# Performance work log

Measured on AMD Instinct MI355X. Metric: run time of the kernel, lower is better.

## Reference

```python
import jax, jax.numpy as jnp
import numpy as np

WINDOW_SIZE = 16


def _gru_seq(x, Wih, Whh, bih, bhh):
    # x: (T, in); Wih: (in, 3H); Whh: (H, 3H); torch gate order r,z,n
    H = Whh.shape[0]
    pre = x @ Wih + bih  # (T, 3H)
    def step(h, pi):
        ph = h @ Whh + bhh
        ri, zi, ni = jnp.split(pi, 3)
        rh, zh, nh = jnp.split(ph, 3)
        r = jax.nn.sigmoid(ri + rh)
        z = jax.nn.sigmoid(zi + zh)
        n = jnp.tanh(ni + r * nh)
        hn = (1.0 - z) * n + z * h
        return hn, hn
    _, ys = jax.lax.scan(step, jnp.zeros((H,), x.dtype), pre)
    return ys


def _bigru(x, Wih, Whh, bih, bhh):
    f = _gru_seq(x, Wih[0], Whh[0], bih[0], bhh[0])
    b = _gru_seq(x[::-1], Wih[1], Whh[1], bih[1], bhh[1])[::-1]
    return jnp.concatenate([f, b], axis=-1)


def setup_inputs() -> dict:
    key = jax.random.key(0)
    ks = iter(jax.random.split(key, 64))
    T, S = 512, 32
    VFD, HID, WED, VOCAB = 1024, 512, 300, 10000
    HH = HID // 2
    def p(*shape):
        return jax.random.normal(next(ks), shape, jnp.float32) * 0.05
    return dict(
        video=jax.random.normal(next(ks), (T, VFD), jnp.float32),
        text=jax.random.randint(next(ks), (S,), 0, VOCAB),
        vp_W=p(VFD, HID), vp_b=p(HID),
        vgru_Wih=p(2, HID, 3 * HH), vgru_Whh=p(2, HH, 3 * HH),
        vgru_bih=p(2, 3 * HH), vgru_bhh=p(2, 3 * HH),
        emb=p(VOCAB, WED),
        tp_W=p(WED, HID), tp_b=p(HID),
        tgru_Wih=p(2, HID, 3 * HH), tgru_Whh=p(2, HH, 3 * HH),
        tgru_bih=p(2, 3 * HH), tgru_bhh=p(2, 3 * HH),
        cma_Wq=p(HID, HID), cma_bq=p(HID), cma_Wk=p(HID, HID), cma_bk=p(HID), cma_v=p(HID),
        cm_gru_Wih=p(2 * HID, 3 * HID), cm_gru_Whh=p(HID, 3 * HID),
        cm_gru_bih=p(3 * HID), cm_gru_bhh=p(3 * HID),
        si_Wq=p(HID, HID), si_bq=p(HID), si_Wk=p(HID, HID), si_bk=p(HID), si_v=p(HID),
        si_gru_Wih=p(2 * HID, 3 * HID), si_gru_Whh=p(HID, 3 * HID),
        si_gru_bih=p(3 * HID), si_gru_bhh=p(3 * HID),
        wp_W1=p(HID, HID), wp_b1=p(HID), wp_v=p(HID),
        cp_W1=p(2 * HID, HID), cp_b1=p(HID), cp_v=p(HID),
    )


def reference(video, text, vp_W, vp_b, vgru_Wih, vgru_Whh, vgru_bih, vgru_bhh,
              emb, tp_W, tp_b, tgru_Wih, tgru_Whh, tgru_bih, tgru_bhh,
              cma_Wq, cma_bq, cma_Wk, cma_bk, cma_v,
              cm_gru_Wih, cm_gru_Whh, cm_gru_bih, cm_gru_bhh,
              si_Wq, si_bq, si_Wk, si_bk, si_v,
              si_gru_Wih, si_gru_Whh, si_gru_bih, si_gru_bhh,
              wp_W1, wp_b1, wp_v, cp_W1, cp_b1, cp_v):
    T = video.shape[0]
    # encoders (dropout is identity in eval)
    H_v = _bigru(video @ vp_W + vp_b, vgru_Wih, vgru_Whh, vgru_bih, vgru_bhh)  # (T, HID)
    H_s = _bigru(emb[text] @ tp_W + tp_b, tgru_Wih, tgru_Whh, tgru_bih, tgru_bhh)  # (S, HID)
    # cross-modal additive attention: score = v . tanh(Wq q + Wk k)
    e = jnp.tanh((H_v @ cma_Wq + cma_bq)[:, None, :] + (H_s @ cma_Wk + cma_bk)[None, :, :])  # (T,S,HID)
    w = jax.nn.softmax(e @ cma_v, axis=1)  # (T,S)
    h_s_bar = w @ H_s  # (T, HID)
    # cross gating (linear layers defined but unused in original forward)
    h_v_t = jax.nn.relu(H_v) * h_s_bar
    h_s_t = jax.nn.relu(h_s_bar) * h_v_t
    h_r = _gru_seq(jnp.concatenate([h_v_t, h_s_t], axis=1),
                   cm_gru_Wih, cm_gru_Whh, cm_gru_bih, cm_gru_bhh)  # (T, HID)
    # self interactor: row i attends over X[i:] -> mask j >= i
    e2 = jnp.tanh((h_r @ si_Wq + si_bq)[:, None, :] + (h_r @ si_Wk + si_bk)[None, :, :])  # (T,T,HID)
    s2 = e2 @ si_v  # (T,T)
    mask = jnp.arange(T)[None, :] >= jnp.arange(T)[:, None]
    s2 = jnp.where(mask, s2, jnp.asarray(-1e30, s2.dtype))
    att = jax.nn.softmax(s2, axis=1) @ h_r  # (T, HID)
    h_d = _gru_seq(jnp.concatenate([h_r, att], axis=1),
                   si_gru_Wih, si_gru_Whh, si_gru_bih, si_gru_bhh)  # (T, HID)
    # segment localizer; torch nn.Softmax() on (S,1) acts on axis=1 (size 1) -> all ones (faithful)
    wlogits = jnp.tanh(H_s @ wp_W1 + wp_b1) @ wp_v  # (S,)
    wts = jax.nn.softmax(wlogits[:, None], axis=1)  # (S,1) == ones
    h_o = jnp.sum(H_s * wts, axis=0)  # (HID,)
    cat = jnp.concatenate([h_d, jnp.broadcast_to(h_o, h_d.shape)], axis=1)  # (T, 2*HID)
    frame_scores = jnp.tanh(cat @ cp_W1 + cp_b1) @ cp_v  # (T,)
    n_win = T - WINDOW_SIZE + 1
    window_starts = jnp.arange(n_win)
    window_scores = frame_scores[:n_win]
    return (window_scores, window_starts)
```

## Files before the change

### kernel.cpp

```cpp
#include <hip/hip_runtime.h>
#include <hip/hip_bf16.h>
#include <cstdint>

#define DEV __device__ __forceinline__

typedef unsigned short ushort;
typedef __attribute__((ext_vector_type(8))) short bf16x8;
typedef __attribute__((ext_vector_type(4))) float f32x4;

DEV float fsig(float x) { return 1.f / (1.f + __expf(-x)); }
DEV float ftanh(float x) { return 1.f - 2.f / (1.f + __expf(2.f * x)); }
DEV ushort f2bu(float f) {
  __hip_bfloat16 h = __float2bfloat16(f);
  return *(ushort*)&h;
}
DEV float b2f(ushort u) { return __uint_as_float((uint32_t)u << 16); }

template <int CTRL>
DEV float dpp_add(float v) {
  int x = __builtin_amdgcn_update_dpp(0, __float_as_int(v), CTRL, 0xF, 0xF, true);
  return v + __int_as_float(x);
}
template <int TPU>
DEV float dpp_reduce(float v) {
  v = dpp_add<0xB1>(v);
  v = dpp_add<0x4E>(v);
  if (TPU >= 8) v = dpp_add<0x141>(v);
  if (TPU >= 16) v = dpp_add<0x140>(v);
  return v;
}

__global__ __launch_bounds__(256)
void mfma_gemm(const ushort* __restrict__ A, const ushort* __restrict__ BT,
               const float* __restrict__ bias, void* __restrict__ Cout,
               int M, int N, int K, int ldc, int flags) {
  const int wave = threadIdx.x >> 6, lane = threadIdx.x & 63;
  const int m0 = blockIdx.y * 64 + wave * 16;
  const int n0 = blockIdx.x * 64;
  const int r = lane & 15, quad = lane >> 4;
  f32x4 acc[4] = {};
  const int arow = (m0 + r < M) ? (m0 + r) : 0;
  const ushort* ap = A + (size_t)arow * K + quad * 8;
  const ushort* bp = BT + (size_t)(n0 + r) * K + quad * 8;
#pragma unroll 2
  for (int k0 = 0; k0 < K; k0 += 32) {
    bf16x8 a = *(const bf16x8*)(ap + k0);
#pragma unroll
    for (int t = 0; t < 4; ++t) {
      bf16x8 b = *(const bf16x8*)(bp + (size_t)t * 16 * K + k0);
      acc[t] = __builtin_amdgcn_mfma_f32_16x16x32_bf16(a, b, acc[t], 0, 0, 0);
    }
  }
#pragma unroll
  for (int t = 0; t < 4; ++t) {
    const int col = n0 + t * 16 + r;
    const float bs = bias ? bias[col] : 0.f;
#pragma unroll
    for (int e = 0; e < 4; ++e) {
      const int row = m0 + quad * 4 + e;
      if (row < M) {
        float v = acc[t][e] + bs;
        if (flags & 1) v = ftanh(v);
        if (flags & 2)
          ((ushort*)Cout)[(size_t)row * ldc + col] = f2bu(v);
        else
          ((float*)Cout)[(size_t)row * ldc + col] = v;
      }
    }
  }
}

struct TDesc {
  const float* src;
  ushort* db;
  float* df;
  int K, N, Kp;
};
struct PrepArgs {
  TDesc d[19];
  int n;
};

__global__ __launch_bounds__(256)
void prep_kernel(PrepArgs pa) {
  int rem = blockIdx.x;
  int di = 0;
  TDesc d{};
  for (; di < pa.n; ++di) {
    d = pa.d[di];
    int t = ((d.N + 31) >> 5) * ((d.Kp + 31) >> 5);
    if (rem < t) break;
    rem -= t;
  }
  if (di == pa.n) return;
  const int ntx = (d.Kp + 31) >> 5;
  const int ty = rem / ntx, tx = rem % ntx;
  __shared__ float t32[32][33];
  const int lx = threadIdx.x & 31, ly = threadIdx.x >> 5;
#pragma unroll
  for (int p = 0; p < 4; ++p) {
    int k = tx * 32 + ly + 8 * p;
    int n = ty * 32 + lx;
    t32[ly + 8 * p][lx] = (k < d.K && n < d.N) ? d.src[(size_t)k * d.N + n] : 0.f;
  }
  __syncthreads();
#pragma unroll
  for (int p = 0; p < 4; ++p) {
    int n = ty * 32 + ly + 8 * p;
    int k = tx * 32 + lx;
    if (n < d.N && k < d.Kp) {
      float v = t32[lx][ly + 8 * p];
      if (d.df)
        d.df[(size_t)n * d.Kp + k] = v;
      else
        d.db[(size_t)n * d.Kp + k] = f2bu(v);
    }
  }
}

__global__ void cast_kernel(const float* __restrict__ in,
                            ushort* __restrict__ out, int n) {
  int i = (blockIdx.x * 256 + threadIdx.x) * 4;
  if (i + 3 < n) {
    float4 v = *(const float4*)(in + i);
    out[i] = f2bu(v.x);
    out[i + 1] = f2bu(v.y);
    out[i + 2] = f2bu(v.z);
    out[i + 3] = f2bu(v.w);
  }
}

__global__ void emb_kernel(const float* __restrict__ emb,
                           const int* __restrict__ text,
                           ushort* __restrict__ xe) {
  int s = blockIdx.x;
  int row = text[s];
  for (int k = threadIdx.x; k < 320; k += 256)
    xe[s * 320 + k] = (k < 300) ? f2bu(emb[(size_t)row * 300 + k]) : (ushort)0;
}

struct ScanDesc {
  const float* whhT;
  const float* bhh;
  const float* pre;
  float* out;
  ushort* outb;
  ushort* outbT;
  uint32_t* hw;
  int T, dir, stride, off, bstride, boff, tld;
};
struct ScanArgs {
  ScanDesc d[4];
};

template <int H, int NB, int TPU>
__global__ __launch_bounds__(H / NB * TPU, 1)
void scan_kernel(ScanArgs args) {
  constexpr int UPB = H / NB;
  constexpr int B = UPB * TPU;
  constexpr int KS = H / TPU;
  constexpr int PP = H / 64;
  const ScanDesc d = args.d[blockIdx.x / NB];
  const int b = blockIdx.x % NB;
  const int tid = threadIdx.x;
  const int slice = tid % TPU, ug = tid / TPU;
  const int unit = b * UPB + ug;
  const int lane = tid & 63;

  float wr[KS], wz[KS], wn[KS];
#pragma unroll
  for (int j2 = 0; j2 < KS / 4; ++j2)
#pragma unroll
    for (int r = 0; r < 4; ++r) {
      int k = slice * 4 + 4 * TPU * j2 + r;
      int j = 4 * j2 + r;
      wr[j] = d.whhT[(size_t)(0 * H + unit) * H + k];
      wz[j] = d.whhT[(size_t)(1 * H + unit) * H + k];
      wn[j] = d.whhT[(size_t)(2 * H + unit) * H + k];
    }
  const float bhr = d.bhh[unit];
  const float bhz = d.bhh[H + unit];
  const float bhn = d.bhh[2 * H + unit];

  __shared__ float hsh[2][H];
  __shared__ int flag;
  for (int i = tid; i < H; i += B) hsh[0][i] = 0.f;
  if (tid == 0) flag = 0;
  __syncthreads();

  const int T = d.T, dir = d.dir, stride = d.stride, off = d.off;
  uint32_t* __restrict__ hwords = d.hw;

  for (int s = 0; s < T; ++s) {
    const int pos = dir ? (T - 1 - s) : s;
    const int cur = s & 1;
    const float* prow = d.pre + (size_t)pos * (3 * H);
    const float pir = prow[unit];
    const float piz = prow[H + unit];
    const float pin = prow[2 * H + unit];

    if (s > 0) {
      const uint32_t want = (uint32_t)s;
      const uint32_t* src = hwords + (size_t)(s - 1) * H + lane;
      for (;;) {
        if (__hip_atomic_load(&flag, __ATOMIC_ACQUIRE,
                              __HIP_MEMORY_SCOPE_WORKGROUP) >= s)
          break;
        uint32_t w[PP];
        bool ok = true;
#pragma unroll
        for (int p = 0; p < PP; ++p)
          w[p] = __hip_atomic_load(src + 64 * p, __ATOMIC_RELAXED,
                                   __HIP_MEMORY_SCOPE_AGENT);
#pragma unroll
        for (int p = 0; p < PP; ++p) ok = ok && ((w[p] >> 16) == want);
        if (__all(ok)) {
#pragma unroll
          for (int p = 0; p < PP; ++p)
            hsh[cur][lane + 64 * p] = b2f((ushort)(w[p] & 0xffffu));
          __hip_atomic_fetch_max(&flag, s, __ATOMIC_RELEASE,
                                 __HIP_MEMORY_SCOPE_WORKGROUP);
          break;
        }
      }
    }

    float ar = 0.f, az = 0.f, an = 0.f;
    const float* hrow = hsh[cur];
#pragma unroll
    for (int j2 = 0; j2 < KS / 4; ++j2) {
      const float4 hv = *(const float4*)&hrow[slice * 4 + 4 * TPU * j2];
      const int j = 4 * j2;
      ar = fmaf(wr[j], hv.x, ar); ar = fmaf(wr[j + 1], hv.y, ar);
      ar = fmaf(wr[j + 2], hv.z, ar); ar = fmaf(wr[j + 3], hv.w, ar);
      az = fmaf(wz[j], hv.x, az); az = fmaf(wz[j + 1], hv.y, az);
      az = fmaf(wz[j + 2], hv.z, az); az = fmaf(wz[j + 3], hv.w, az);
      an = fmaf(wn[j], hv.x, an); an = fmaf(wn[j + 1], hv.y, an);
      an = fmaf(wn[j + 2], hv.z, an); an = fmaf(wn[j + 3], hv.w, an);
    }
    ar = dpp_reduce<TPU>(ar);
    az = dpp_reduce<TPU>(az);
    an = dpp_reduce<TPU>(an);

    if (slice == 0) {
      const float hp = hrow[unit];
      float r = fsig(pir + ar + bhr);
      float z = fsig(piz + az + bhz);
      float n = ftanh(pin + r * (an + bhn));
      float hn = (1.f - z) * n + z * hp;
      const ushort hb = f2bu(hn);
      d.out[(size_t)pos * stride + off + unit] = hn;
      if (d.outb) d.outb[(size_t)pos * d.bstride + d.boff + unit] = hb;
      if (d.outbT) d.outbT[(size_t)unit * d.tld + pos] = hb;
      uint32_t wv = ((uint32_t)(s + 1) << 16) | (uint32_t)hb;
      __hip_atomic_store(&hwords[(size_t)s * H + unit], wv, __ATOMIC_RELAXED,
                         __HIP_MEMORY_SCOPE_AGENT);
    }
  }
}

__global__ __launch_bounds__(256)
void cma_kernel(const ushort* __restrict__ qv, const ushort* __restrict__ ksm,
                const float* __restrict__ cmav, const float* __restrict__ Hv,
                const float* __restrict__ Hs, ushort* __restrict__ Xcm) {
  const int t = blockIdx.x, tid = threadIdx.x;
  const int lane = tid & 63, wave = tid >> 6;
  __shared__ float qsh[512], vsh[512], wsm[32];
  qsh[tid] = b2f(qv[t * 512 + tid]);
  qsh[256 + tid] = b2f(qv[t * 512 + 256 + tid]);
  vsh[tid] = cmav[tid];
  vsh[256 + tid] = cmav[256 + tid];
  __syncthreads();
  for (int s = wave; s < 32; s += 4) {
    float p = 0.f;
#pragma unroll
    for (int j = 0; j < 8; ++j) {
      int c = lane + 64 * j;
      p += ftanh(qsh[c] + b2f(ksm[s * 512 + c])) * vsh[c];
    }
#pragma unroll
    for (int m = 32; m >= 1; m >>= 1) p += __shfl_xor(p, m, 64);
    if (lane == 0) wsm[s] = p;
  }
  __syncthreads();
  float mx = -1e30f;
  for (int s = 0; s < 32; ++s) mx = fmaxf(mx, wsm[s]);
  float sum = 0.f;
  for (int s = 0; s < 32; ++s) sum += __expf(wsm[s] - mx);
  float inv = 1.f / sum;
  __syncthreads();
  if (tid < 32) wsm[tid] = __expf(wsm[tid] - mx) * inv;
  __syncthreads();
#pragma unroll
  for (int rep = 0; rep < 2; ++rep) {
    int c = tid + 256 * rep;
    float acc = 0.f;
#pragma unroll
    for (int s = 0; s < 32; ++s) acc += wsm[s] * Hs[s * 512 + c];
    float hb = acc;
    float hv = fmaxf(Hv[(size_t)t * 512 + c], 0.f) * hb;
    float hs2 = fmaxf(hb, 0.f) * hv;
    Xcm[(size_t)t * 1024 + c] = f2bu(hv);
    Xcm[(size_t)t * 1024 + 512 + c] = f2bu(hs2);
  }
}

__global__ __launch_bounds__(256)
void selfatt_score(const ushort* __restrict__ q2, const ushort* __restrict__ k2,
                   const float* __restrict__ siv, const ushort* __restrict__ hrb,
                   ushort* __restrict__ P, ushort* __restrict__ Xsi) {
  const int i = blockIdx.x, tid = threadIdx.x;
  const int lane = tid & 63, wave = tid >> 6;
  __shared__ float qsh[512], vsh[512], scr[512];
  qsh[tid] = b2f(q2[(size_t)i * 512 + tid]);
  qsh[256 + tid] = b2f(q2[(size_t)i * 512 + 256 + tid]);
  vsh[tid] = siv[tid];
  vsh[256 + tid] = siv[256 + tid];
  Xsi[(size_t)i * 1024 + tid] = hrb[(size_t)i * 512 + tid];
  Xsi[(size_t)i * 1024 + 256 + tid] = hrb[(size_t)i * 512 + 256 + tid];
  __syncthreads();
  for (int j = i + wave; j < 512; j += 4) {
    float p = 0.f;
#pragma unroll
    for (int r = 0; r < 8; ++r) {
      int c = lane + 64 * r;
      p += ftanh(qsh[c] + b2f(k2[(size_t)j * 512 + c])) * vsh[c];
    }
#pragma unroll
    for (int m = 32; m >= 1; m >>= 1) p += __shfl_xor(p, m, 64);
    if (lane == 0) scr[j] = p;
  }
  __syncthreads();
  float mx = -1e30f;
  for (int j = i; j < 512; ++j) mx = fmaxf(mx, scr[j]);
  float sum = 0.f;
  for (int j = i; j < 512; ++j) sum += __expf(scr[j] - mx);
  float inv = 1.f / sum;
  __syncthreads();
  for (int j = tid; j < 512; j += 256) {
    float p = (j >= i) ? __expf(scr[j] - mx) * inv : 0.f;
    P[(size_t)i * 512 + j] = f2bu(p);
  }
}

__global__ void ho_kernel(const float* __restrict__ Hs, float* __restrict__ ho) {
  int c = blockIdx.x * 256 + threadIdx.x;
  float a = 0.f;
#pragma unroll
  for (int s = 0; s < 32; ++s) a += Hs[s * 512 + c];
  ho[c] = a;
}

__global__ void cat_kernel(const float* __restrict__ hd,
                           const float* __restrict__ ho,
                           ushort* __restrict__ cat) {
  int i = blockIdx.x, tid = threadIdx.x;
#pragma unroll
  for (int r = 0; r < 4; ++r) {
    int k = tid + 256 * r;
    float v = (k < 512) ? hd[(size_t)i * 512 + k] : ho[k - 512];
    cat[(size_t)i * 1024 + k] = f2bu(v);
  }
}

__global__ __launch_bounds__(256)
void score_kernel(const float* __restrict__ tmp, const float* __restrict__ cpv,
                  float* __restrict__ out) {
  const int i = blockIdx.x, tid = threadIdx.x;
  float p = tmp[(size_t)i * 512 + tid] * cpv[tid] +
            tmp[(size_t)i * 512 + 256 + tid] * cpv[256 + tid];
#pragma unroll
  for (int m = 32; m >= 1; m >>= 1) p += __shfl_xor(p, m, 64);
  __shared__ float wsum[4];
  if ((tid & 63) == 0) wsum[tid >> 6] = p;
  __syncthreads();
  if (tid == 0) {
    out[i] = wsum[0] + wsum[1] + wsum[2] + wsum[3];
    out[497 + i] = (float)i;
  }
}

extern "C" void kernel_launch(void* const* d_in, const int* in_sizes, int n_in,
                              void* d_out, int out_size, void* d_ws,
                              size_t ws_size, hipStream_t stream) {
  const float* video = (const float*)d_in[0];
  const int* text = (const int*)d_in[1];
  const float* vp_W = (const float*)d_in[2];
  const float* vp_b = (const float*)d_in[3];
  const float* vWih = (const float*)d_in[4];
  const float* vWhh = (const float*)d_in[5];
  const float* vbih = (const float*)d_in[6];
  const float* vbhh = (const float*)d_in[7];
  const float* emb = (const float*)d_in[8];
  const float* tp_W = (const float*)d_in[9];
  const float* tp_b = (const float*)d_in[10];
  const float* tWih = (const float*)d_in[11];
  const float* tWhh = (const float*)d_in[12];
  const float* tbih = (const float*)d_in[13];
  const float* tbhh = (const float*)d_in[14];
  const float* cmaWq = (const float*)d_in[15];
  const float* cmabq = (const float*)d_in[16];
  const float* cmaWk = (const float*)d_in[17];
  const float* cmabk = (const float*)d_in[18];
  const float* cmav = (const float*)d_in[19];
  const float* cmWih = (const float*)d_in[20];
  const float* cmWhh = (const float*)d_in[21];
  const float* cmbih = (const float*)d_in[22];
  const float* cmbhh = (const float*)d_in[23];
  const float* siWq = (const float*)d_in[24];
  const float* sibq = (const float*)d_in[25];
  const float* siWk = (const float*)d_in[26];
  const float* sibk = (const float*)d_in[27];
  const float* siv = (const float*)d_in[28];
  const float* sgWih = (const float*)d_in[29];
  const float* sgWhh = (const float*)d_in[30];
  const float* sgbih = (const float*)d_in[31];
  const float* sgbhh = (const float*)d_in[32];
  const float* cpW1 = (const float*)d_in[36];
  const float* cpb1 = (const float*)d_in[37];
  const float* cpv = (const float*)d_in[38];
  float* out = (float*)d_out;

  float* ws = (float*)d_ws;
  size_t off = 0;
  auto alloc = [&](size_t n) {
    float* p = ws + off;
    off += (n + 3) & ~(size_t)3;
    return p;
  };
  auto allocU = [&](size_t n) { return (ushort*)alloc((n + 1) / 2); };
  ushort* video_b = allocU(512 * 1024);
  ushort* x_emb_b = allocU(32 * 320);
  ushort* x_v_b = allocU(512 * 512);
  ushort* x_s_b = allocU(32 * 512);
  float* pre_v = alloc(2 * 512 * 768);
  float* pre_s = alloc(2 * 32 * 768);
  float* Hv = alloc(512 * 512);
  ushort* Hv_b = allocU(512 * 512);
  float* Hs = alloc(32 * 512);
  ushort* Hs_b = allocU(32 * 512);
  ushort* qv_b = allocU(512 * 512);
  ushort* ksb_b = allocU(32 * 512);
  ushort* Xcm_b = allocU(512 * 1024);
  float* pre_cm = alloc(512 * 1536);
  float* hr = alloc(512 * 512);
  ushort* hr_b = allocU(512 * 512);
  ushort* hrT_b = allocU(512 * 512);
  ushort* q2_b = allocU(512 * 512);
  ushort* k2_b = allocU(512 * 512);
  ushort* P_b = allocU(512 * 512);
  ushort* Xsi_b = allocU(512 * 1024);
  float* pre_si = alloc(512 * 1536);
  float* hd = alloc(512 * 512);
  float* ho = alloc(512);
  ushort* cat_b = allocU(512 * 1024);
  float* tmpb = alloc(512 * 512);
  float* whhT_v = alloc(2 * 768 * 256);
  float* whhT_t = alloc(2 * 768 * 256);
  float* whhT_cm = alloc(1536 * 512);
  float* whhT_si = alloc(1536 * 512);
  ushort* vpW_T = allocU(512 * 1024);
  ushort* vWihT_f = allocU(768 * 512);
  ushort* vWihT_b = allocU(768 * 512);
  ushort* tpW_T = allocU(512 * 320);
  ushort* tWihT_f = allocU(768 * 512);
  ushort* tWihT_b = allocU(768 * 512);
  ushort* cmaWqT = allocU(512 * 512);
  ushort* cmaWkT = allocU(512 * 512);
  ushort* cmWihT = allocU(1536 * 1024);
  ushort* siWqT = allocU(512 * 512);
  ushort* siWkT = allocU(512 * 512);
  ushort* sgWihT = allocU(1536 * 1024);
  ushort* cpW1T = allocU(512 * 1024);
  float* zero0 = ws + off;
  uint32_t* hw_vf = (uint32_t*)alloc(512 * 256);
  uint32_t* hw_vb = (uint32_t*)alloc(512 * 256);
  uint32_t* hw_tf = (uint32_t*)alloc(32 * 256);
  uint32_t* hw_tb = (uint32_t*)alloc(32 * 256);
  uint32_t* hw_cm = (uint32_t*)alloc(512 * 512);
  uint32_t* hw_si = (uint32_t*)alloc(512 * 512);
  size_t zero_bytes = ((ws + off) - zero0) * sizeof(float);
  hipMemsetAsync(zero0, 0, zero_bytes, stream);

  PrepArgs pa{};
  int nd = 0;
  size_t total_tiles = 0;
  auto addT = [&](const float* src, ushort* db, float* df, int K, int N, int Kp) {
    pa.d[nd++] = TDesc{src, db, df, K, N, Kp};
    total_tiles += (size_t)((N + 31) / 32) * ((Kp + 31) / 32);
  };
  addT(vWhh, nullptr, whhT_v, 256, 768, 256);
  addT(vWhh + 196608, nullptr, whhT_v + 196608, 256, 768, 256);
  addT(tWhh, nullptr, whhT_t, 256, 768, 256);
  addT(tWhh + 196608, nullptr, whhT_t + 196608, 256, 768, 256);
  addT(cmWhh, nullptr, whhT_cm, 512, 1536, 512);
  addT(sgWhh, nullptr, whhT_si, 512, 1536, 512);
  addT(vp_W, vpW_T, nullptr, 1024, 512, 1024);
  addT(vWih, vWihT_f, nullptr, 512, 768, 512);
  addT(vWih + 393216, vWihT_b, nullptr, 512, 768, 512);
  addT(tp_W, tpW_T, nullptr, 300, 512, 320);
  addT(tWih, tWihT_f, nullptr, 512, 768, 512);
  addT(tWih + 393216, tWihT_b, nullptr, 512, 768, 512);
  addT(cmaWq, cmaWqT, nullptr, 512, 512, 512);
  addT(cmaWk, cmaWkT, nullptr, 512, 512, 512);
  addT(cmWih, cmWihT, nullptr, 1024, 1536, 1024);
  addT(siWq, siWqT, nullptr, 512, 512, 512);
  addT(siWk, siWkT, nullptr, 512, 512, 512);
  addT(sgWih, sgWihT, nullptr, 1024, 1536, 1024);
  addT(cpW1, cpW1T, nullptr, 1024, 512, 1024);
  pa.n = nd;
  prep_kernel<<<(int)total_tiles, 256, 0, stream>>>(pa);

  cast_kernel<<<512, 256, 0, stream>>>(video, video_b, 512 * 1024);
  emb_kernel<<<32, 256, 0, stream>>>(emb, text, x_emb_b);

  mfma_gemm<<<dim3(8, 8), 256, 0, stream>>>(video_b, vpW_T, vp_b, x_v_b, 512, 512, 1024, 512, 2);
  mfma_gemm<<<dim3(12, 8), 256, 0, stream>>>(x_v_b, vWihT_f, vbih, pre_v, 512, 768, 512, 768, 0);
  mfma_gemm<<<dim3(12, 8), 256, 0, stream>>>(x_v_b, vWihT_b, vbih + 768, pre_v + 393216, 512, 768, 512, 768, 0);
  mfma_gemm<<<dim3(8, 1), 256, 0, stream>>>(x_emb_b, tpW_T, tp_b, x_s_b, 32, 512, 320, 512, 2);
  mfma_gemm<<<dim3(12, 1), 256, 0, stream>>>(x_s_b, tWihT_f, tbih, pre_s, 32, 768, 512, 768, 0);
  mfma_gemm<<<dim3(12, 1), 256, 0, stream>>>(x_s_b, tWihT_b, tbih + 768, pre_s + 24576, 32, 768, 512, 768, 0);

  ScanArgs a1{};
  a1.d[0] = ScanDesc{whhT_v, vbhh, pre_v, Hv, Hv_b, nullptr, hw_vf, 512, 0, 512, 0, 512, 0, 0};
  a1.d[1] = ScanDesc{whhT_v + 196608, vbhh + 768, pre_v + 393216, Hv, Hv_b, nullptr, hw_vb, 512, 1, 512, 256, 512, 256, 0};
  a1.d[2] = ScanDesc{whhT_t, tbhh, pre_s, Hs, Hs_b, nullptr, hw_tf, 32, 0, 512, 0, 512, 0, 0};
  a1.d[3] = ScanDesc{whhT_t + 196608, tbhh + 768, pre_s + 24576, Hs, Hs_b, nullptr, hw_tb, 32, 1, 512, 256, 512, 256, 0};
  scan_kernel<256, 8, 8><<<32, 256, 0, stream>>>(a1);

  mfma_gemm<<<dim3(8, 8), 256, 0, stream>>>(Hv_b, cmaWqT, cmabq, qv_b, 512, 512, 512, 512, 2);
  mfma_gemm<<<dim3(8, 1), 256, 0, stream>>>(Hs_b, cmaWkT, cmabk, ksb_b, 32, 512, 512, 512, 2);
  cma_kernel<<<512, 256, 0, stream>>>(qv_b, ksb_b, cmav, Hv, Hs, Xcm_b);
  mfma_gemm<<<dim3(24, 8), 256, 0, stream>>>(Xcm_b, cmWihT, cmbih, pre_cm, 512, 1536, 1024, 1536, 0);

  ScanArgs a2{};
  a2.d[0] = ScanDesc{whhT_cm, cmbhh, pre_cm, hr, hr_b, hrT_b, hw_cm, 512, 0, 512, 0, 512, 0, 512};
  scan_kernel<512, 32, 16><<<32, 256, 0, stream>>>(a2);

  mfma_gemm<<<dim3(8, 8), 256, 0, stream>>>(hr_b, siWqT, sibq, q2_b, 512, 512, 512, 512, 2);
  mfma_gemm<<<dim3(8, 8), 256, 0, stream>>>(hr_b, siWkT, sibk, k2_b, 512, 512, 512, 512, 2);
  selfatt_score<<<512, 256, 0, stream>>>(q2_b, k2_b, siv, hr_b, P_b, Xsi_b);
  mfma_gemm<<<dim3(8, 8), 256, 0, stream>>>(P_b, hrT_b, nullptr, Xsi_b + 512, 512, 512, 512, 1024, 2);
  mfma_gemm<<<dim3(24, 8), 256, 0, stream>>>(Xsi_b, sgWihT, sgbih, pre_si, 512, 1536, 1024, 1536, 0);

  ScanArgs a3{};
  a3.d[0] = ScanDesc{whhT_si, sgbhh, pre_si, hd, nullptr, nullptr, hw_si, 512, 0, 512, 0, 0, 0, 0};
  scan_kernel<512, 32, 16><<<32, 256, 0, stream>>>(a3);

  ho_kernel<<<2, 256, 0, stream>>>(Hs, ho);
  cat_kernel<<<512, 256, 0, stream>>>(hd, ho, cat_b);
  mfma_gemm<<<dim3(8, 8), 256, 0, stream>>>(cat_b, cpW1T, cpb1, tmpb, 512, 512, 1024, 512, 1);
  score_kernel<<<497, 256, 0, stream>>>(tmpb, cpv, out);
}
```

Baseline: 3.916 ms.

## Co-locate scan workgroups on one XCD and use L2-coherent sc0 polling

Launches 256 blocks for each GRU scan. The first 32 blocks to land on a single XCD claim the work slots and the rest exit. Because all cooperating blocks then share one L2, a runtime test checks that sc0 stores are visible to the other blocks; if so, the per-step hidden-state exchange uses sc0 loads and stores instead of agent-scope atomics, which is meant to cut cross-XCD coherence latency on the serial path. Polling is restricted to wave 0, and the other waves spin on an LDS flag. The change adds a launch-time election and handshake, relies on undocumented hardware-register and cache behaviour, and falls back to a slow-path check every 16 poll rounds.

```diff
diff --git a/kernel.cpp b/kernel.cpp
--- a/kernel.cpp
+++ b/kernel.cpp
@@ -28,6 +28,54 @@
   if (TPU >= 8) v = dpp_add<0x141>(v);
   if (TPU >= 16) v = dpp_add<0x140>(v);
   return v;
+}
+
+DEV int get_xcd() {
+  int x;
+  asm volatile("s_getreg_b32 %0, hwreg(20, 0, 32)" : "=s"(x));
+  return x & 7;
+}
+
+DEV void store_sc0_u32(uint32_t* p, uint32_t v) {
+  asm volatile("global_store_dword %0, %1, off sc0" ::"v"(p), "v"(v) : "memory");
+}
+DEV uint32_t load_sc0_u32(const uint32_t* p) {
+  uint32_t v;
+  asm volatile("global_load_dword %0, %1, off sc0\ns_waitcnt vmcnt(0)"
+               : "=v"(v) : "v"(p) : "memory");
+  return v;
+}
+template <int PP>
+DEV void fast_poll32(const uint32_t* p, uint32_t (&v)[PP]);
+template <>
+DEV void fast_poll32<4>(const uint32_t* p, uint32_t (&v)[4]) {
+  asm volatile(
+      "global_load_dword %0, %4, off sc0\n\t"
+      "global_load_dword %1, %5, off sc0\n\t"
+      "global_load_dword %2, %6, off sc0\n\t"
+      "global_load_dword %3, %7, off sc0\n\t"
+      "s_waitcnt vmcnt(0)"
+      : "=&v"(v[0]), "=&v"(v[1]), "=&v"(v[2]), "=&v"(v[3])
+      : "v"(p), "v"(p + 64), "v"(p + 128), "v"(p + 192)
+      : "memory");
+}
+template <>
+DEV void fast_poll32<8>(const uint32_t* p, uint32_t (&v)[8]) {
+  asm volatile(
+      "global_load_dword %0, %8, off sc0\n\t"
+      "global_load_dword %1, %9, off sc0\n\t"
+      "global_load_dword %2, %10, off sc0\n\t"
+      "global_load_dword %3, %11, off sc0\n\t"
+      "global_load_dword %4, %12, off sc0\n\t"
+      "global_load_dword %5, %13, off sc0\n\t"
+      "global_load_dword %6, %14, off sc0\n\t"
+      "global_load_dword %7, %15, off sc0\n\t"
+      "s_waitcnt vmcnt(0)"
+      : "=&v"(v[0]), "=&v"(v[1]), "=&v"(v[2]), "=&v"(v[3]), "=&v"(v[4]),
+        "=&v"(v[5]), "=&v"(v[6]), "=&v"(v[7])
+      : "v"(p), "v"(p + 64), "v"(p + 128), "v"(p + 192), "v"(p + 256),
+        "v"(p + 320), "v"(p + 384), "v"(p + 448)
+      : "memory");
 }
 
 __global__ __launch_bounds__(256)
@@ -146,26 +194,88 @@
   float* out;
   ushort* outb;
   ushort* outbT;
-  uint32_t* hw;
+  uint32_t* hwS;
+  uint32_t* hwF;
   int T, dir, stride, off, bstride, boff, tld;
 };
 struct ScanArgs {
   ScanDesc d[4];
+  uint32_t* ctrl;
 };
 
-template <int H, int NB, int TPU>
-__global__ __launch_bounds__(H / NB * TPU, 1)
+template <int H, int NB, int TPU, int NINST>
+__global__ __launch_bounds__(256, 1)
 void scan_kernel(ScanArgs args) {
   constexpr int UPB = H / NB;
   constexpr int B = UPB * TPU;
   constexpr int KS = H / TPU;
   constexpr int PP = H / 64;
-  const ScanDesc d = args.d[blockIdx.x / NB];
-  const int b = blockIdx.x % NB;
+  constexpr int W = NB * NINST;
   const int tid = threadIdx.x;
+
+  __shared__ int sh_slot, sh_fast;
+  if (tid == 0) {
+    uint32_t* c = args.ctrl;
+    const int x = get_xcd();
+    int slot = (int)__hip_atomic_fetch_add(&c[x], 1u, __ATOMIC_RELAXED,
+                                           __HIP_MEMORY_SCOPE_AGENT);
+    if (slot == W - 1) atomicCAS((unsigned*)&c[8], 0u, (unsigned)(x + 1));
+    unsigned win;
+    while ((win = __hip_atomic_load(&c[8], __ATOMIC_RELAXED,
+                                    __HIP_MEMORY_SCOPE_AGENT)) == 0) {}
+    const bool work = ((int)win == x + 1) && slot < W;
+    int fast = 0;
+    if (work) {
+      store_sc0_u32(&c[144 + slot], 0xC0FFEEu);
+      __hip_atomic_store(&c[80 + slot], 1u, __ATOMIC_RELAXED,
+                         __HIP_MEMORY_SCOPE_AGENT);
+      for (;;) {
+        bool all = true;
+#pragma unroll
+        for (int i = 0; i < W; ++i)
+          all = all && (__hip_atomic_load(&c[80 + i], __ATOMIC_RELAXED,
+                                          __HIP_MEMORY_SCOPE_AGENT) != 0);
+        if (all) break;
+      }
+      int ok = 0;
+      for (int r = 0; r < 128 && !ok; ++r) {
+        bool all = true;
+#pragma unroll
+        for (int i = 0; i < W; ++i)
+          all = all && (load_sc0_u32(&c[144 + i]) == 0xC0FFEEu);
+        if (all) ok = 1;
+      }
+      __hip_atomic_store(&c[16 + slot], ok ? 1u : 2u, __ATOMIC_RELAXED,
+                         __HIP_MEMORY_SCOPE_AGENT);
+      if (slot == 0) {
+        uint32_t g = 1;
+        for (int i = 0; i < W; ++i) {
+          uint32_t v;
+          while ((v = __hip_atomic_load(&c[16 + i], __ATOMIC_RELAXED,
+                                        __HIP_MEMORY_SCOPE_AGENT)) == 0) {}
+          if (v != 1) g = 2;
+        }
+        __hip_atomic_store(&c[12], g, __ATOMIC_RELAXED,
+                           __HIP_MEMORY_SCOPE_AGENT);
+      }
+      uint32_t g;
+      while ((g = __hip_atomic_load(&c[12], __ATOMIC_RELAXED,
+                                    __HIP_MEMORY_SCOPE_AGENT)) == 0) {}
+      fast = (g == 1);
+    }
+    sh_slot = work ? slot : -1;
+    sh_fast = fast;
+  }
+  __syncthreads();
+  const int slot = sh_slot;
+  if (slot < 0) return;
+  const bool fastmode = (sh_fast != 0);
+
+  const ScanDesc d = args.d[slot / NB];
+  const int b = slot % NB;
   const int slice = tid % TPU, ug = tid / TPU;
   const int unit = b * UPB + ug;
-  const int lane = tid & 63;
+  const int wid = tid >> 6, lane = tid & 63;
 
   float wr[KS], wz[KS], wn[KS];
 #pragma unroll
@@ -189,7 +299,8 @@
   __syncthreads();
 
   const int T = d.T, dir = d.dir, stride = d.stride, off = d.off;
-  uint32_t* __restrict__ hwords = d.hw;
+  uint32_t* __restrict__ hwS = d.hwS;
+  uint32_t* __restrict__ hwF = d.hwF;
 
   for (int s = 0; s < T; ++s) {
     const int pos = dir ? (T - 1 - s) : s;
@@ -200,28 +311,51 @@
     const float pin = prow[2 * H + unit];
 
     if (s > 0) {
-      const uint32_t want = (uint32_t)s;
-      const uint32_t* src = hwords + (size_t)(s - 1) * H + lane;
-      for (;;) {
-        if (__hip_atomic_load(&flag, __ATOMIC_ACQUIRE,
-                              __HIP_MEMORY_SCOPE_WORKGROUP) >= s)
-          break;
+      if (wid == 0) {
+        const uint32_t want = (uint32_t)s;
+        const uint32_t* fsrc = hwF + (size_t)(s - 1) * H + lane;
+        const uint32_t* ssrc = hwS + (size_t)(s - 1) * H + lane;
         uint32_t w[PP];
-        bool ok = true;
+        if (fastmode) {
+          int rounds = 0;
+          for (;;) {
+            fast_poll32<PP>(fsrc, w);
+            bool ok = true;
+#pragma unroll
+            for (int p = 0; p < PP; ++p) ok = ok && ((w[p] >> 16) == want);
+            if (__all(ok)) break;
+            if ((++rounds & 15) == 0) {
+              bool ok2 = true;
+#pragma unroll
+              for (int p = 0; p < PP; ++p)
+                w[p] = __hip_atomic_load(ssrc + 64 * p, __ATOMIC_RELAXED,
+                                         __HIP_MEMORY_SCOPE_AGENT);
+#pragma unroll
+              for (int p = 0; p < PP; ++p)
+                ok2 = ok2 && ((w[p] >> 16) == want);
+              if (__all(ok2)) break;
+            }
+          }
+        } else {
+          for (;;) {
+            bool ok = true;
+#pragma unroll
+            for (int p = 0; p < PP; ++p)
+              w[p] = __hip_atomic_load(ssrc + 64 * p, __ATOMIC_RELAXED,
+                                       __HIP_MEMORY_SCOPE_AGENT);
+#pragma unroll
+            for (int p = 0; p < PP; ++p) ok = ok && ((w[p] >> 16) == want);
+            if (__all(ok)) break;
+          }
+        }
 #pragma unroll
         for (int p = 0; p < PP; ++p)
-          w[p] = __hip_atomic_load(src + 64 * p, __ATOMIC_RELAXED,
-                                   __HIP_MEMORY_SCOPE_AGENT);
-#pragma unroll
-        for (int p = 0; p < PP; ++p) ok = ok && ((w[p] >> 16) == want);
-        if (__all(ok)) {
-#pragma unroll
-          for (int p = 0; p < PP; ++p)
-            hsh[cur][lane + 64 * p] = b2f((ushort)(w[p] & 0xffffu));
-          __hip_atomic_fetch_max(&flag, s, __ATOMIC_RELEASE,
-                                 __HIP_MEMORY_SCOPE_WORKGROUP);
-          break;
-        }
+          hsh[cur][lane + 64 * p] = b2f((ushort)(w[p] & 0xffffu));
+        __hip_atomic_store(&flag, s, __ATOMIC_RELEASE,
+                           __HIP_MEMORY_SCOPE_WORKGROUP);
+      } else {
+        while (__hip_atomic_load(&flag, __ATOMIC_ACQUIRE,
+                                 __HIP_MEMORY_SCOPE_WORKGROUP) < s) {}
       }
     }
 
@@ -253,7 +387,8 @@
       if (d.outb) d.outb[(size_t)pos * d.bstride + d.boff + unit] = hb;
       if (d.outbT) d.outbT[(size_t)unit * d.tld + pos] = hb;
       uint32_t wv = ((uint32_t)(s + 1) << 16) | (uint32_t)hb;
-      __hip_atomic_store(&hwords[(size_t)s * H + unit], wv, __ATOMIC_RELAXED,
+      if (fastmode) store_sc0_u32(&hwF[(size_t)s * H + unit], wv);
+      __hip_atomic_store(&hwS[(size_t)s * H + unit], wv, __ATOMIC_RELAXED,
                          __HIP_MEMORY_SCOPE_AGENT);
     }
   }
@@ -473,12 +608,21 @@
   ushort* sgWihT = allocU(1536 * 1024);
   ushort* cpW1T = allocU(512 * 1024);
   float* zero0 = ws + off;
-  uint32_t* hw_vf = (uint32_t*)alloc(512 * 256);
-  uint32_t* hw_vb = (uint32_t*)alloc(512 * 256);
-  uint32_t* hw_tf = (uint32_t*)alloc(32 * 256);
-  uint32_t* hw_tb = (uint32_t*)alloc(32 * 256);
-  uint32_t* hw_cm = (uint32_t*)alloc(512 * 512);
-  uint32_t* hw_si = (uint32_t*)alloc(512 * 512);
+  uint32_t* hwS_vf = (uint32_t*)alloc(512 * 256);
+  uint32_t* hwS_vb = (uint32_t*)alloc(512 * 256);
+  uint32_t* hwS_tf = (uint32_t*)alloc(32 * 256);
+  uint32_t* hwS_tb = (uint32_t*)alloc(32 * 256);
+  uint32_t* hwS_cm = (uint32_t*)alloc(512 * 512);
+  uint32_t* hwS_si = (uint32_t*)alloc(512 * 512);
+  uint32_t* hwF_vf = (uint32_t*)alloc(512 * 256);
+  uint32_t* hwF_vb = (uint32_t*)alloc(512 * 256);
+  uint32_t* hwF_tf = (uint32_t*)alloc(32 * 256);
+  uint32_t* hwF_tb = (uint32_t*)alloc(32 * 256);
+  uint32_t* hwF_cm = (uint32_t*)alloc(512 * 512);
+  uint32_t* hwF_si = (uint32_t*)alloc(512 * 512);
+  uint32_t* ctrl1 = (uint32_t*)alloc(256);
+  uint32_t* ctrl2 = (uint32_t*)alloc(256);
+  uint32_t* ctrl3 = (uint32_t*)alloc(256);
   size_t zero_bytes = ((ws + off) - zero0) * sizeof(float);
   hipMemsetAsync(zero0, 0, zero_bytes, stream);
 
@@ -522,11 +666,12 @@
   mfma_gemm<<<dim3(12, 1), 256, 0, stream>>>(x_s_b, tWihT_b, tbih + 768, pre_s + 24576, 32, 768, 512, 768, 0);
 
   ScanArgs a1{};
-  a1.d[0] = ScanDesc{whhT_v, vbhh, pre_v, Hv, Hv_b, nullptr, hw_vf, 512, 0, 512, 0, 512, 0, 0};
-  a1.d[1] = ScanDesc{whhT_v + 196608, vbhh + 768, pre_v + 393216, Hv, Hv_b, nullptr, hw_vb, 512, 1, 512, 256, 512, 256, 0};
-  a1.d[2] = ScanDesc{whhT_t, tbhh, pre_s, Hs, Hs_b, nullptr, hw_tf, 32, 0, 512, 0, 512, 0, 0};
-  a1.d[3] = ScanDesc{whhT_t + 196608, tbhh + 768, pre_s + 24576, Hs, Hs_b, nullptr, hw_tb, 32, 1, 512, 256, 512, 256, 0};
-  scan_kernel<256, 8, 8><<<32, 256, 0, stream>>>(a1);
+  a1.d[0] = ScanDesc{whhT_v, vbhh, pre_v, Hv, Hv_b, nullptr, hwS_vf, hwF_vf, 512, 0, 512, 0, 512, 0, 0};
+  a1.d[1] = ScanDesc{whhT_v + 196608, vbhh + 768, pre_v + 393216, Hv, Hv_b, nullptr, hwS_vb, hwF_vb, 512, 1, 512, 256, 512, 256, 0};
+  a1.d[2] = ScanDesc{whhT_t, tbhh, pre_s, Hs, Hs_b, nullptr, hwS_tf, hwF_tf, 32, 0, 512, 0, 512, 0, 0};
+  a1.d[3] = ScanDesc{whhT_t + 196608, tbhh + 768, pre_s + 24576, Hs, Hs_b, nullptr, hwS_tb, hwF_tb, 32, 1, 512, 256, 512, 256, 0};
+  a1.ctrl = ctrl1;
+  scan_kernel<256, 8, 8, 4><<<256, 256, 0, stream>>>(a1);
 
   mfma_gemm<<<dim3(8, 8), 256, 0, stream>>>(Hv_b, cmaWqT, cmabq, qv_b, 512, 512, 512, 512, 2);
   mfma_gemm<<<dim3(8, 1), 256, 0, stream>>>(Hs_b, cmaWkT, cmabk, ksb_b, 32, 512, 512, 512, 2);
@@ -534,8 +679,9 @@
   mfma_gemm<<<dim3(24, 8), 256, 0, stream>>>(Xcm_b, cmWihT, cmbih, pre_cm, 512, 1536, 1024, 1536, 0);
 
   ScanArgs a2{};
-  a2.d[0] = ScanDesc{whhT_cm, cmbhh, pre_cm, hr, hr_b, hrT_b, hw_cm, 512, 0, 512, 0, 512, 0, 512};
-  scan_kernel<512, 32, 16><<<32, 256, 0, stream>>>(a2);
+  a2.d[0] = ScanDesc{whhT_cm, cmbhh, pre_cm, hr, hr_b, hrT_b, hwS_cm, hwF_cm, 512, 0, 512, 0, 512, 0, 512};
+  a2.ctrl = ctrl2;
+  scan_kernel<512, 32, 16, 1><<<256, 256, 0, stream>>>(a2);
 
   mfma_gemm<<<dim3(8, 8), 256, 0, stream>>>(hr_b, siWqT, sibq, q2_b, 512, 512, 512, 512, 2);
   mfma_gemm<<<dim3(8, 8), 256, 0, stream>>>(hr_b, siWkT, sibk, k2_b, 512, 512, 512, 512, 2);
@@ -544,8 +690,9 @@
   mfma_gemm<<<dim3(24, 8), 256, 0, stream>>>(Xsi_b, sgWihT, sgbih, pre_si, 512, 1536, 1024, 1536, 0);
 
   ScanArgs a3{};
-  a3.d[0] = ScanDesc{whhT_si, sgbhh, pre_si, hd, nullptr, nullptr, hw_si, 512, 0, 512, 0, 0, 0, 0};
-  scan_kernel<512, 32, 16><<<32, 256, 0, stream>>>(a3);
+  a3.d[0] = ScanDesc{whhT_si, sgbhh, pre_si, hd, nullptr, nullptr, hwS_si, hwF_si, 512, 0, 512, 0, 0, 0, 0};
+  a3.ctrl = ctrl3;
+  scan_kernel<512, 32, 16, 1><<<256, 256, 0, stream>>>(a3);
 
   ho_kernel<<<2, 256, 0, stream>>>(Hs, ho);
   cat_kernel<<<512, 256, 0, stream>>>(hd, ho, cat_b);
```

Measured after the change: 5.851 ms. 49.4% more time.

## Poll cross-block hidden state with one wave, publish state before outputs

Applied to the files above, without the earlier changes.

In the recurrent scan kernel, only wave 0 now spins on the global hidden-state words from other blocks. The other waves sleep-wait on a shared-memory flag, so the block no longer sends redundant global polling traffic from every wave. Each step's hidden-state word is stored before the output writes so downstream blocks see it sooner. Unused fp32 outputs of the two big scans are dropped, and cat_kernel reads the bf16 copy directly. The s_sleep can add wake-up latency on the critical serial path.

```diff
diff --git a/kernel.cpp b/kernel.cpp
--- a/kernel.cpp
+++ b/kernel.cpp
@@ -154,7 +154,7 @@
 };
 
 template <int H, int NB, int TPU>
-__global__ __launch_bounds__(H / NB * TPU, 1)
+__global__ __launch_bounds__(256, 1)
 void scan_kernel(ScanArgs args) {
   constexpr int UPB = H / NB;
   constexpr int B = UPB * TPU;
@@ -165,7 +165,7 @@
   const int tid = threadIdx.x;
   const int slice = tid % TPU, ug = tid / TPU;
   const int unit = b * UPB + ug;
-  const int lane = tid & 63;
+  const int wid = tid >> 6, lane = tid & 63;
 
   float wr[KS], wz[KS], wn[KS];
 #pragma unroll
@@ -189,7 +189,7 @@
   __syncthreads();
 
   const int T = d.T, dir = d.dir, stride = d.stride, off = d.off;
-  uint32_t* __restrict__ hwords = d.hw;
+  uint32_t* __restrict__ hw = d.hw;
 
   for (int s = 0; s < T; ++s) {
     const int pos = dir ? (T - 1 - s) : s;
@@ -200,28 +200,29 @@
     const float pin = prow[2 * H + unit];
 
     if (s > 0) {
-      const uint32_t want = (uint32_t)s;
-      const uint32_t* src = hwords + (size_t)(s - 1) * H + lane;
-      for (;;) {
-        if (__hip_atomic_load(&flag, __ATOMIC_ACQUIRE,
-                              __HIP_MEMORY_SCOPE_WORKGROUP) >= s)
-          break;
+      if (wid == 0) {
+        const uint32_t want = (uint32_t)s;
+        const uint32_t* src = hw + (size_t)(s - 1) * H + lane;
         uint32_t w[PP];
-        bool ok = true;
+        for (;;) {
+          bool ok = true;
+#pragma unroll
+          for (int p = 0; p < PP; ++p)
+            w[p] = __hip_atomic_load(src + 64 * p, __ATOMIC_RELAXED,
+                                     __HIP_MEMORY_SCOPE_AGENT);
+#pragma unroll
+          for (int p = 0; p < PP; ++p) ok = ok && ((w[p] >> 16) == want);
+          if (__all(ok)) break;
+        }
 #pragma unroll
         for (int p = 0; p < PP; ++p)
-          w[p] = __hip_atomic_load(src + 64 * p, __ATOMIC_RELAXED,
-                                   __HIP_MEMORY_SCOPE_AGENT);
-#pragma unroll
-        for (int p = 0; p < PP; ++p) ok = ok && ((w[p] >> 16) == want);
-        if (__all(ok)) {
-#pragma unroll
-          for (int p = 0; p < PP; ++p)
-            hsh[cur][lane + 64 * p] = b2f((ushort)(w[p] & 0xffffu));
-          __hip_atomic_fetch_max(&flag, s, __ATOMIC_RELEASE,
-                                 __HIP_MEMORY_SCOPE_WORKGROUP);
-          break;
-        }
+          hsh[cur][lane + 64 * p] = b2f((ushort)(w[p] & 0xffffu));
+        __hip_atomic_store(&flag, s, __ATOMIC_RELEASE,
+                           __HIP_MEMORY_SCOPE_WORKGROUP);
+      } else {
+        while (__hip_atomic_load(&flag, __ATOMIC_ACQUIRE,
+                                 __HIP_MEMORY_SCOPE_WORKGROUP) < s)
+          __builtin_amdgcn_s_sleep(1);
       }
     }
 
@@ -249,12 +250,12 @@
       float n = ftanh(pin + r * (an + bhn));
       float hn = (1.f - z) * n + z * hp;
       const ushort hb = f2bu(hn);
-      d.out[(size_t)pos * stride + off + unit] = hn;
+      uint32_t wv = ((uint32_t)(s + 1) << 16) | (uint32_t)hb;
+      __hip_atomic_store(&hw[(size_t)s * H + unit], wv, __ATOMIC_RELAXED,
+                         __HIP_MEMORY_SCOPE_AGENT);
+      if (d.out) d.out[(size_t)pos * stride + off + unit] = hn;
       if (d.outb) d.outb[(size_t)pos * d.bstride + d.boff + unit] = hb;
       if (d.outbT) d.outbT[(size_t)unit * d.tld + pos] = hb;
-      uint32_t wv = ((uint32_t)(s + 1) << 16) | (uint32_t)hb;
-      __hip_atomic_store(&hwords[(size_t)s * H + unit], wv, __ATOMIC_RELAXED,
-                         __HIP_MEMORY_SCOPE_AGENT);
     }
   }
 }
@@ -351,15 +352,15 @@
   ho[c] = a;
 }
 
-__global__ void cat_kernel(const float* __restrict__ hd,
+__global__ void cat_kernel(const ushort* __restrict__ hdb,
                            const float* __restrict__ ho,
                            ushort* __restrict__ cat) {
   int i = blockIdx.x, tid = threadIdx.x;
 #pragma unroll
   for (int r = 0; r < 4; ++r) {
     int k = tid + 256 * r;
-    float v = (k < 512) ? hd[(size_t)i * 512 + k] : ho[k - 512];
-    cat[(size_t)i * 1024 + k] = f2bu(v);
+    cat[(size_t)i * 1024 + k] =
+        (k < 512) ? hdb[(size_t)i * 512 + k] : f2bu(ho[k - 512]);
   }
 }
 
@@ -443,7 +444,6 @@
   ushort* ksb_b = allocU(32 * 512);
   ushort* Xcm_b = allocU(512 * 1024);
   float* pre_cm = alloc(512 * 1536);
-  float* hr = alloc(512 * 512);
   ushort* hr_b = allocU(512 * 512);
   ushort* hrT_b = allocU(512 * 512);
   ushort* q2_b = allocU(512 * 512);
@@ -451,7 +451,7 @@
   ushort* P_b = allocU(512 * 512);
   ushort* Xsi_b = allocU(512 * 1024);
   float* pre_si = alloc(512 * 1536);
-  float* hd = alloc(512 * 512);
+  ushort* hd_b = allocU(512 * 512);
   float* ho = alloc(512);
   ushort* cat_b = allocU(512 * 1024);
   float* tmpb = alloc(512 * 512);
@@ -534,7 +534,7 @@
   mfma_gemm<<<dim3(24, 8), 256, 0, stream>>>(Xcm_b, cmWihT, cmbih, pre_cm, 512, 1536, 1024, 1536, 0);
 
   ScanArgs a2{};
-  a2.d[0] = ScanDesc{whhT_cm, cmbhh, pre_cm, hr, hr_b, hrT_b, hw_cm, 512, 0, 512, 0, 512, 0, 512};
+  a2.d[0] = ScanDesc{whhT_cm, cmbhh, pre_cm, nullptr, hr_b, hrT_b, hw_cm, 512, 0, 0, 0, 512, 0, 512};
   scan_kernel<512, 32, 16><<<32, 256, 0, stream>>>(a2);
 
   mfma_gemm<<<dim3(8, 8), 256, 0, stream>>>(hr_b, siWqT, sibq, q2_b, 512, 512, 512, 512, 2);
@@ -544,11 +544,11 @@
   mfma_gemm<<<dim3(24, 8), 256, 0, stream>>>(Xsi_b, sgWihT, sgbih, pre_si, 512, 1536, 1024, 1536, 0);
 
   ScanArgs a3{};
-  a3.d[0] = ScanDesc{whhT_si, sgbhh, pre_si, hd, nullptr, nullptr, hw_si, 512, 0, 512, 0, 0, 0, 0};
+  a3.d[0] = ScanDesc{whhT_si, sgbhh, pre_si, nullptr, hd_b, nullptr, hw_si, 512, 0, 0, 0, 512, 0, 0};
   scan_kernel<512, 32, 16><<<32, 256, 0, stream>>>(a3);
 
   ho_kernel<<<2, 256, 0, stream>>>(Hs, ho);
-  cat_kernel<<<512, 256, 0, stream>>>(hd, ho, cat_b);
+  cat_kernel<<<512, 256, 0, stream>>>(hd_b, ho, cat_b);
   mfma_gemm<<<dim3(8, 8), 256, 0, stream>>>(cat_b, cpW1T, cpb1, tmpb, 512, 512, 1024, 512, 1);
   score_kernel<<<497, 256, 0, stream>>>(tmpb, cpv, out);
 }
```

New measurement: 4.076 ms. 1.04x slower.
